# Kernel optimization log

Measured on AMD Instinct MI355X. Metric: run time of the kernel, lower is better.

Reference implementation:

```python
import math
import jax, jax.numpy as jnp
import numpy as np

C, H, W = 128, 64, 64
R, K = 7, 3          # 7x3 dilated window
PAD_H, PAD_W = 9, 2  # from unfold paddings
DIL_H, DIL_W = 3, 2  # row/col dilations


def _neighborhood(x):
    """Gather dilated 7x3 neighborhood: out[n,c,r,k,i,j] = x[n,c, i+3r-9, j+2k-2] (zero-padded).
    x: (n,c,h,w) -> (n,c,7,3,h,w)."""
    n, c, h, w = x.shape
    xp = jnp.pad(x, ((0, 0), (0, 0), (PAD_H, PAD_H), (PAD_W, PAD_W)))
    taps = [xp[:, :, DIL_H * r:DIL_H * r + h, DIL_W * k:DIL_W * k + w]
            for r in range(R) for k in range(K)]
    return jnp.stack(taps, axis=2).reshape(n, c, R, K, h, w)


def setup_inputs() -> dict:
    key = jax.random.key(0)
    k1, k2, k3 = jax.random.split(key, 3)
    x = jax.random.normal(k1, (4, C, H, W), dtype=jnp.float32)
    p5_w = 0.1 * jax.random.normal(k2, (1, C, R, K, H, W), dtype=jnp.float32)
    p6_w = 0.1 * jax.random.normal(k3, (1, C, R, K, C), dtype=jnp.float32)
    return {"x": x, "p5_w": p5_w, "p6_w": p6_w}


def reference(x, p5_w, p6_w):
    n, c, h, w = x.shape
    # t_2: dilated 7x3 neighborhood gather (double unfold)
    t2 = _neighborhood(x)                                   # (n,c,7,3,h,w)
    # t_3: bmm((n,c*21,hw), (n,hw,c)) / sqrt(hw)
    t3 = jnp.einsum('ncrkhw,ndhw->ncrkd', t2, x) / math.sqrt(h * w)  # (n,c,7,3,c)
    # elementwise modulation
    t7 = p5_w * t2 + t2                                     # (n,c,7,3,h,w)
    t6 = p6_w * t3                                          # (n,c,7,3,c)
    # t_8: bmm((n,hw,c*21), (n,c*21,c)) / sqrt(c*21)
    t8 = jnp.einsum('ncrkhw,ncrkd->nhwd', t7, t6) / math.sqrt(c * R * K)  # (n,h,w,c)
    return jnp.transpose(t8, (0, 3, 1, 2))                  # (n,c,h,w)
```

## Files before the change

### kernel.cpp

```cpp
#include <hip/hip_runtime.h>

typedef _Float16 f16;
typedef _Float16 f16x2 __attribute__((ext_vector_type(2)));
typedef _Float16 f16x4 __attribute__((ext_vector_type(4)));
typedef _Float16 f16x8 __attribute__((ext_vector_type(8)));
typedef float    f32x4 __attribute__((ext_vector_type(4)));

#define XROWS 82
#define XSTR  (XROWS * 64)
#define XK_ELEMS (3u * 4u * 128u * (unsigned)XSTR)
static const size_t T6T_OFF   = (size_t)XK_ELEMS * 2;
static const size_t T6T_BYTES = (size_t)4 * 128 * 2688 * 2;
static const size_t T3P_OFF   = T6T_OFF + T6T_BYTES;
static const size_t T8P_OFF   = T3P_OFF;

__device__ __forceinline__ void gl16(const f16* g, f16* l) {
  __builtin_amdgcn_global_load_lds((const __attribute__((address_space(1))) void*)g,
                                   (__attribute__((address_space(3))) void*)l, 16, 0, 0);
}

__global__ __launch_bounds__(256) void prep_kernel(const float* __restrict__ x,
                                                   f16* __restrict__ xk) {
  unsigned p = blockIdx.x * 256u + threadIdx.x;
  unsigned total = 3u * 4u * 128u * 82u * 32u;
  if (p >= total) return;
  unsigned wp   = p & 31u;
  unsigned row  = (p >> 5) % 82u;
  unsigned rest = p / (32u * 82u);
  unsigned c    = rest & 127u;
  unsigned rest2 = rest >> 7;
  unsigned n    = rest2 & 3u;
  unsigned kc   = rest2 >> 2;
  int hsrc = (int)row - 9;
  int wsrc = (int)(wp * 2u) + 2 * (int)kc - 2;
  f16x2 v; v.x = (f16)0.f; v.y = (f16)0.f;
  if (hsrc >= 0 && hsrc < 64 && wsrc >= 0 && wsrc < 64) {
    const float2* src = (const float2*)(x + (((size_t)(n * 128u + c) * 64u + (unsigned)hsrc) * 64u + (unsigned)wsrc));
    float2 xv = *src;
    v.x = (f16)(xv.x * 0.125f);
    v.y = (f16)(xv.y * 0.125f);
  }
  ((f16x2*)xk)[p] = v;
}

__global__ __launch_bounds__(256, 3) void gram_kernel(const f16* __restrict__ xk,
                                                      f16* __restrict__ t3p) {
  __shared__ f16 gl[2 * 12288];

  unsigned b    = blockIdx.x;
  unsigned ks   = b & 7u;
  unsigned cseg = (b >> 3) & 1u;
  unsigned rki  = (b >> 4) % 11u;
  unsigned n    = b / 176u;
  unsigned r    = rki / 3u;
  unsigned kc   = rki - r * 3u;

  unsigned tid  = threadIdx.x;
  unsigned wv   = tid >> 6;
  unsigned lane = tid & 63u;
  unsigned wy   = wv >> 1;
  unsigned wx   = wv & 1u;
  unsigned quad = lane >> 4;
  unsigned l16  = lane & 15u;
  unsigned rsl  = lane >> 3;
  unsigned seg  = (lane & 7u) ^ (rsl & 7u);

  unsigned h0 = ks * 8u;
  const f16* Ab = xk + (size_t)(kc * 4u + n) * 128u * XSTR + (size_t)(cseg * 64u) * XSTR
                + (h0 + 3u * r) * 64u + seg * 8u;
  const f16* Bb = xk + (size_t)(4u + n) * 128u * XSTR + (h0 + 9u) * 64u + seg * 8u;
  unsigned ar0 = wv * 16u;
  unsigned br0 = wv * 32u;

  f32x4 acc[2][4] = {};

#pragma unroll
  for (unsigned t = 0; t < 2u; t++)
    gl16(Ab + (size_t)(ar0 + t * 8u + rsl) * XSTR, &gl[(ar0 + t * 8u) * 64u]);
#pragma unroll
  for (unsigned t = 0; t < 4u; t++)
    gl16(Bb + (size_t)(br0 + t * 8u + rsl) * XSTR, &gl[4096u + (br0 + t * 8u) * 64u]);

  for (unsigned s = 0; s < 8u; s++) {
    __syncthreads();
    if (s < 7u) {
      f16* base = &gl[((s + 1u) & 1u) * 12288u];
      unsigned off = (s + 1u) * 64u;
#pragma unroll
      for (unsigned t = 0; t < 2u; t++)
        gl16(Ab + off + (size_t)(ar0 + t * 8u + rsl) * XSTR, base + (ar0 + t * 8u) * 64u);
#pragma unroll
      for (unsigned t = 0; t < 4u; t++)
        gl16(Bb + off + (size_t)(br0 + t * 8u + rsl) * XSTR, base + 4096u + (br0 + t * 8u) * 64u);
    }
    const f16* bufA = &gl[(s & 1u) * 12288u];
    const f16* bufB = bufA + 4096u;
#pragma unroll
    for (unsigned t2 = 0; t2 < 2u; t2++) {
      unsigned L = t2 * 4u + quad;
      f16x8 a[2], bb[4];
#pragma unroll
      for (int ms = 0; ms < 2; ms++) {
        unsigned rr = wy * 32u + (unsigned)ms * 16u + l16;
        a[ms] = *(const f16x8*)&bufA[rr * 64u + (L ^ (rr & 7u)) * 8u];
      }
#pragma unroll
      for (int ns = 0; ns < 4; ns++) {
        unsigned rb = wx * 64u + (unsigned)ns * 16u + l16;
        bb[ns] = *(const f16x8*)&bufB[rb * 64u + (L ^ (rb & 7u)) * 8u];
      }
#pragma unroll
      for (int ms = 0; ms < 2; ms++)
#pragma unroll
        for (int ns = 0; ns < 4; ns++)
          acc[ms][ns] = __builtin_amdgcn_mfma_f32_16x16x32_f16(a[ms], bb[ns], acc[ms][ns], 0, 0, 0);
    }
  }

  f16* tp = t3p + ((size_t)(ks * 4u + n) * 11u + rki) * 16384u;
#pragma unroll
  for (int ms = 0; ms < 2; ms++) {
#pragma unroll
    for (int ns = 0; ns < 4; ns++) {
      unsigned c0 = cseg * 64u + wy * 32u + (unsigned)ms * 16u + quad * 4u;
      unsigned d  = wx * 64u + (unsigned)ns * 16u + l16;
#pragma unroll
      for (int reg = 0; reg < 4; reg++)
        tp[(size_t)(c0 + (unsigned)reg) * 128u + d] = (f16)acc[ms][ns][reg];
    }
  }
}

__global__ __launch_bounds__(256) void ep_kernel(const f16* __restrict__ t3p,
                                                 const float* __restrict__ p6,
                                                 f16* __restrict__ t6B) {
  unsigned idx = blockIdx.x * 256u + threadIdx.x;
  unsigned t   = idx >> 12;
  unsigned rk  = t % 21u;
  unsigned n   = t / 21u;
  f16* tb = t6B + (size_t)t * 16384u;

  if (rk <= 10u) {
    unsigned d4 = idx & 31u;
    unsigned c  = (idx >> 5) & 127u;
    unsigned d0 = d4 * 4u;
    float s0 = 0.f, s1 = 0.f, s2 = 0.f, s3 = 0.f;
#pragma unroll
    for (unsigned ks = 0; ks < 8u; ks++) {
      f16x4 v = *(const f16x4*)(t3p + (((size_t)(ks * 4u + n) * 11u + rk) * 16384u + c * 128u + d0));
      s0 += (float)v[0]; s1 += (float)v[1]; s2 += (float)v[2]; s3 += (float)v[3];
    }
    const float* pp = p6 + ((size_t)c * 21u + rk) * 128u + d0;
    f16* ob = tb + (c >> 5) * 4096u + (d0 >> 4) * 512u + ((c >> 3) & 3u) * 128u + (d0 & 15u) * 8u + (c & 7u);
    ob[0]  = (f16)(s0 * pp[0]);
    ob[8]  = (f16)(s1 * pp[1]);
    ob[16] = (f16)(s2 * pp[2]);
    ob[24] = (f16)(s3 * pp[3]);
  } else {
    unsigned mrk = 20u - rk;
    unsigned c4 = idx & 31u;
    unsigned d  = (idx >> 5) & 127u;
    unsigned c0 = c4 * 4u;
    float s0 = 0.f, s1 = 0.f, s2 = 0.f, s3 = 0.f;
#pragma unroll
    for (unsigned ks = 0; ks < 8u; ks++) {
      f16x4 v = *(const f16x4*)(t3p + (((size_t)(ks * 4u + n) * 11u + mrk) * 16384u + d * 128u + c0));
      s0 += (float)v[0]; s1 += (float)v[1]; s2 += (float)v[2]; s3 += (float)v[3];
    }
    f16x4 o;
    o[0] = (f16)(s0 * p6[((size_t)(c0 + 0u) * 21u + rk) * 128u + d]);
    o[1] = (f16)(s1 * p6[((size_t)(c0 + 1u) * 21u + rk) * 128u + d]);
    o[2] = (f16)(s2 * p6[((size_t)(c0 + 2u) * 21u + rk) * 128u + d]);
    o[3] = (f16)(s3 * p6[((size_t)(c0 + 3u) * 21u + rk) * 128u + d]);
    *(f16x4*)(tb + (c0 >> 5) * 4096u + (d >> 4) * 512u + ((c0 >> 3) & 3u) * 128u + (d & 15u) * 8u + (c0 & 7u)) = o;
  }
}

#define RT_STR   66
__global__ __launch_bounds__(512, 8) void outp_kernel(const f16* __restrict__ xk,
                                                      const float* __restrict__ p5,
                                                      const f16* __restrict__ t6B,
                                                      f16* __restrict__ t8p) {
  __shared__ float smem[8448];
  f16* sm16 = (f16*)smem;

  unsigned b = blockIdx.x;
  unsigned g = b & 3u;
  unsigned h = (b >> 2) & 63u;
  unsigned n = b >> 8;

  unsigned tid  = threadIdx.x;
  unsigned wv   = tid >> 6;
  unsigned lane = tid & 63u;
  unsigned wy   = wv >> 2;
  unsigned wx   = wv & 3u;
  unsigned quad = lane >> 4;
  unsigned l16  = lane & 15u;
  unsigned wst  = tid & 63u;
  bool     stg  = (tid < 256u);
  unsigned cg8  = tid >> 6;
  unsigned cth  = g * 32u + cg8 * 8u;

  const float* prow0 = p5 + (size_t)cth * (21u * 4096u) + h * 64u + wst;
  const f16* t6base = t6B + (size_t)n * 344064u + g * 4096u;

  f32x4 acc[2][2] = {};
  f16x8 avE, avO;

  auto refill = [&](unsigned rk, f16x8& av) {
    unsigned rr  = rk / 3u;
    unsigned kcc = rk - rr * 3u;
    const f16* xrow = xk + (((size_t)(kcc * 4u + n) * 128u + cth) * XROWS + (h + 3u * rr)) * 64u + wst;
    const float* prow = prow0 + rk * 4096u;
#pragma unroll
    for (int i = 0; i < 8; i++)
      av[i] = (f16)((float)xrow[(size_t)i * XSTR] * (1.0f + prow[(size_t)i * (21u * 4096u)]));
  };

  {
    if (stg) { refill(0u, avE); refill(1u, avO); }
    gl16(t6base + (size_t)tid * 8u, sm16 + 4096u + tid * 8u);
  }

#define OUTP_BODY(J, AVC, BUFC)                                                         \
  {                                                                                     \
    f16* Ag = sm16 + (BUFC) * 2048u;                                                    \
    const f16* Bg = sm16 + 4096u + (BUFC) * 4096u;                                      \
    if (stg) {                                                                          \
      unsigned gw = ((wst & 1u) << 2) | cg8;                                            \
      *(f16x8*)&Ag[(wst >> 1) * 64u + (gw ^ ((wst >> 1) & 7u)) * 8u] = AVC;             \
    }                                                                                   \
    __syncthreads();                                                                    \
    if ((J) < 20u)                                                                      \
      gl16(t6base + (size_t)((J) + 1u) * 16384u + tid * 8u,                             \
           sm16 + 4096u + (1u - (BUFC)) * 4096u + tid * 8u);                            \
    if ((J) + 2u <= 20u && stg) refill((J) + 2u, AVC);                                  \
    f16x8 a[2], bfr[2];                                                                 \
    _Pragma("unroll")                                                                   \
    for (int ms = 0; ms < 2; ms++) {                                                    \
      unsigned rr = wy * 32u + (unsigned)ms * 16u + l16;                                \
      unsigned gr2 = ((rr & 1u) << 2) | quad;                                           \
      a[ms] = *(const f16x8*)&Ag[(rr >> 1) * 64u + (gr2 ^ ((rr >> 1) & 7u)) * 8u];      \
    }                                                                                   \
    _Pragma("unroll")                                                                   \
    for (int ns = 0; ns < 2; ns++)                                                      \
      bfr[ns] = *(const f16x8*)&Bg[(wx * 2u + (unsigned)ns) * 512u + lane * 8u];        \
    _Pragma("unroll")                                                                   \
    for (int ms = 0; ms < 2; ms++)                                                      \
      _Pragma("unroll")                                                                 \
      for (int ns = 0; ns < 2; ns++)                                                    \
        acc[ms][ns] = __builtin_amdgcn_mfma_f32_16x16x32_f16(a[ms], bfr[ns], acc[ms][ns], 0, 0, 0); \
  }

  for (unsigned jp = 0; jp < 10u; jp++) {
    unsigned j0 = jp * 2u;
    OUTP_BODY(j0,       avE, 0u)
    OUTP_BODY(j0 + 1u,  avO, 1u)
  }
  OUTP_BODY(20u, avE, 0u)
#undef OUTP_BODY

  __syncthreads();
  float* Rt = smem;
#pragma unroll
  for (int ms = 0; ms < 2; ms++)
#pragma unroll
    for (int ns = 0; ns < 2; ns++) {
      unsigned w0 = wy * 32u + (unsigned)ms * 16u + quad * 4u;
      unsigned d  = wx * 32u + (unsigned)ns * 16u + l16;
#pragma unroll
      for (int reg = 0; reg < 4; reg++)
        Rt[d * RT_STR + w0 + (unsigned)reg] = acc[ms][ns][reg];
    }
  __syncthreads();
  f16* op = t8p + ((size_t)((g * 4u + n) * 64u + h)) * 8192u;
  {
    unsigned row = tid >> 2;
    unsigned w0  = (tid & 3u) * 16u;
    f16x8 o0, o1;
#pragma unroll
    for (int i = 0; i < 8; i++) {
      o0[i] = (f16)Rt[row * RT_STR + w0 + (unsigned)i];
      o1[i] = (f16)Rt[row * RT_STR + w0 + 8u + (unsigned)i];
    }
    *(f16x8*)(op + row * 64u + w0) = o0;
    *(f16x8*)(op + row * 64u + w0 + 8u) = o1;
  }
}

__global__ __launch_bounds__(256) void red_kernel(const f16* __restrict__ t8p,
                                                  float* __restrict__ out) {
  unsigned idx = blockIdx.x * 256u + threadIdx.x;
  unsigned w0 = (idx & 7u) * 8u;
  unsigned h  = (idx >> 3) & 63u;
  unsigned d  = (idx >> 9) & 127u;
  unsigned n  = idx >> 16;
  const float FS = 0.15430334996209192f;
  float s[8] = {};
#pragma unroll
  for (unsigned g = 0; g < 4u; g++) {
    f16x8 v = *(const f16x8*)(t8p + ((size_t)((g * 4u + n) * 64u + h)) * 8192u + d * 64u + w0);
#pragma unroll
    for (int i = 0; i < 8; i++) s[i] += (float)v[i];
  }
  f32x4 o0, o1;
#pragma unroll
  for (int i = 0; i < 4; i++) { o0[i] = s[i] * FS; o1[i] = s[i + 4] * FS; }
  float* op = out + ((size_t)(n * 128u + d) * 64u + h) * 64u + w0;
  *(f32x4*)op = o0;
  *(f32x4*)(op + 4) = o1;
}

extern "C" void kernel_launch(void* const* d_in, const int* in_sizes, int n_in,
                              void* d_out, int out_size, void* d_ws, size_t ws_size,
                              hipStream_t stream) {
  const float* x  = (const float*)d_in[0];
  const float* p5 = (const float*)d_in[1];
  const float* p6 = (const float*)d_in[2];
  float* out = (float*)d_out;
  f16* xk  = (f16*)((char*)d_ws);
  f16* t6B = (f16*)((char*)d_ws + T6T_OFF);
  f16* t3p = (f16*)((char*)d_ws + T3P_OFF);
  f16* t8p = (f16*)((char*)d_ws + T8P_OFF);

  unsigned prep_blocks = (3u * 4u * 128u * 82u * 32u + 255u) / 256u;
  hipLaunchKernelGGL(prep_kernel, dim3(prep_blocks), dim3(256), 0, stream, x, xk);
  hipLaunchKernelGGL(gram_kernel, dim3(704),  dim3(256), 0, stream, xk, t3p);
  hipLaunchKernelGGL(ep_kernel,   dim3(1344), dim3(256), 0, stream, t3p, p6, t6B);
  hipLaunchKernelGGL(outp_kernel, dim3(1024), dim3(512), 0, stream, xk, p5, t6B, t8p);
  hipLaunchKernelGGL(red_kernel,  dim3(1024), dim3(256), 0, stream, t8p, out);
}
```

Before: 150.1 us.

## Defer modulation math and use partial vmcnt waits to keep loads in flight

The outp kernel now issues raw x and p5 global loads for step J+2 and delays the (1+p5)*x multiply and fp16 conversion until that step's LDS store. The full __syncthreads is replaced by explicit s_waitcnt vmcnt(16) plus s_barrier, so the prefetched register loads stay outstanding across the barrier while only the async LDS copy completes. Scheduling barriers fix the instruction order and the occupancy hint drops from 8 to 6 to make room for the extra live registers. The hand-counted vmcnt value has to match the real number of outstanding loads, and lower occupancy may reduce latency hiding.

```diff
diff --git a/kernel.cpp b/kernel.cpp
--- a/kernel.cpp
+++ b/kernel.cpp
@@ -177,7 +177,7 @@
 }
 
 #define RT_STR   66
-__global__ __launch_bounds__(512, 8) void outp_kernel(const f16* __restrict__ xk,
+__global__ __launch_bounds__(512, 6) void outp_kernel(const f16* __restrict__ xk,
                                                       const float* __restrict__ p5,
                                                       const f16* __restrict__ t6B,
                                                       f16* __restrict__ t8p) {
@@ -205,36 +205,58 @@
   const f16* t6base = t6B + (size_t)n * 344064u + g * 4096u;
 
   f32x4 acc[2][2] = {};
-  f16x8 avE, avO;
-
-  auto refill = [&](unsigned rk, f16x8& av) {
-    unsigned rr  = rk / 3u;
-    unsigned kcc = rk - rr * 3u;
-    const f16* xrow = xk + (((size_t)(kcc * 4u + n) * 128u + cth) * XROWS + (h + 3u * rr)) * 64u + wst;
-    const float* prow = prow0 + rk * 4096u;
-#pragma unroll
-    for (int i = 0; i < 8; i++)
-      av[i] = (f16)((float)xrow[(size_t)i * XSTR] * (1.0f + prow[(size_t)i * (21u * 4096u)]));
-  };
+  f16x8 xvE, xvO; float pvE[8], pvO[8];
 
   {
-    if (stg) { refill(0u, avE); refill(1u, avO); }
     gl16(t6base + (size_t)tid * 8u, sm16 + 4096u + tid * 8u);
-  }
-
-#define OUTP_BODY(J, AVC, BUFC)                                                         \
+    __builtin_amdgcn_sched_barrier(0);
+    if (stg) {
+      const f16* xr0 = xk + (((size_t)n * 128u + cth) * XROWS + h) * 64u + wst;
+      const f16* xr1 = xk + (((size_t)(1u * 4u + n) * 128u + cth) * XROWS + h) * 64u + wst;
+#pragma unroll
+      for (int i = 0; i < 8; i++) {
+        xvE[i] = xr0[(size_t)i * XSTR]; pvE[i] = prow0[(size_t)i * (21u * 4096u)];
+      }
+#pragma unroll
+      for (int i = 0; i < 8; i++) {
+        xvO[i] = xr1[(size_t)i * XSTR]; pvO[i] = prow0[4096u + (size_t)i * (21u * 4096u)];
+      }
+    }
+  }
+
+#define OUTP_BODY(J, XVC, PVC, BUFC)                                                    \
   {                                                                                     \
     f16* Ag = sm16 + (BUFC) * 2048u;                                                    \
     const f16* Bg = sm16 + 4096u + (BUFC) * 4096u;                                      \
     if (stg) {                                                                          \
+      f16x8 av;                                                                         \
+      _Pragma("unroll")                                                                 \
+      for (int i = 0; i < 8; i++)                                                       \
+        av[i] = (f16)((float)XVC[i] * (1.0f + PVC[i]));                                 \
       unsigned gw = ((wst & 1u) << 2) | cg8;                                            \
-      *(f16x8*)&Ag[(wst >> 1) * 64u + (gw ^ ((wst >> 1) & 7u)) * 8u] = AVC;             \
+      *(f16x8*)&Ag[(wst >> 1) * 64u + (gw ^ ((wst >> 1) & 7u)) * 8u] = av;              \
+      if ((J) < 20u) { asm volatile("s_waitcnt vmcnt(16) lgkmcnt(0)" ::: "memory"); }   \
+      else           { asm volatile("s_waitcnt vmcnt(0) lgkmcnt(0)" ::: "memory"); }    \
+    } else {                                                                            \
+      asm volatile("s_waitcnt vmcnt(0) lgkmcnt(0)" ::: "memory");                       \
     }                                                                                   \
-    __syncthreads();                                                                    \
+    __builtin_amdgcn_s_barrier();                                                       \
+    __builtin_amdgcn_sched_barrier(0);                                                  \
     if ((J) < 20u)                                                                      \
       gl16(t6base + (size_t)((J) + 1u) * 16384u + tid * 8u,                             \
            sm16 + 4096u + (1u - (BUFC)) * 4096u + tid * 8u);                            \
-    if ((J) + 2u <= 20u && stg) refill((J) + 2u, AVC);                                  \
+    __builtin_amdgcn_sched_barrier(0);           \
+    if ((J) + 2u <= 20u && stg) {                                                       \
+      unsigned rk = (J) + 2u;                                                           \
+      unsigned rr = rk / 3u;                                                            \
+      unsigned kcc = rk - rr * 3u;                                                      \
+      const f16* xrow = xk + (((size_t)(kcc * 4u + n) * 128u + cth) * XROWS + (h + 3u * rr)) * 64u + wst; \
+      const float* prow = prow0 + rk * 4096u;                                           \
+      _Pragma("unroll")                                                                 \
+      for (int i = 0; i < 8; i++) {                                                     \
+        XVC[i] = xrow[(size_t)i * XSTR]; PVC[i] = prow[(size_t)i * (21u * 4096u)];      \
+      }                                                                                 \
+    }                                                                                   \
     f16x8 a[2], bfr[2];                                                                 \
     _Pragma("unroll")                                                                   \
     for (int ms = 0; ms < 2; ms++) {                                                    \
@@ -254,10 +276,10 @@
 
   for (unsigned jp = 0; jp < 10u; jp++) {
     unsigned j0 = jp * 2u;
-    OUTP_BODY(j0,       avE, 0u)
-    OUTP_BODY(j0 + 1u,  avO, 1u)
-  }
-  OUTP_BODY(20u, avE, 0u)
+    OUTP_BODY(j0,       xvE, pvE, 0u)
+    OUTP_BODY(j0 + 1u,  xvO, pvO, 1u)
+  }
+  OUTP_BODY(20u, xvE, pvE, 0u)
 #undef OUTP_BODY
 
   __syncthreads();
```

Measured after the change: 191.7 us. +27.8%, slower.
